# Performance work log

Hardware: AMD Instinct MI355X
Metric: run time of the kernel (lower is better)

The kernel has to match this reference:

```python
import jax, jax.numpy as jnp
import numpy as np

NUM_PHONES = 39
BLANK = NUM_PHONES  # blank appended as last class
NEG = -1e30  # finite stand-in for -inf (log-space)


def ctc_loss(lp, targets, input_lengths, target_lengths, blank):
    """lp: (T, B, C) log-probs. Returns torch-style CTCLoss(reduction='mean', zero_infinity=True)."""
    T, B, C = lp.shape
    L = targets.shape[1]
    S = 2 * L + 1
    # extended label sequence: blank, l1, blank, l2, ..., blank
    ext = jnp.full((B, S), blank, dtype=targets.dtype).at[:, 1::2].set(targets)
    ext_m2 = jnp.concatenate([jnp.full((B, 2), blank, dtype=ext.dtype), ext[:, :-2]], axis=1)
    skip = (ext != blank) & (ext != ext_m2)  # (B, S) allow s-2 transition
    # per-step emission log-probs gathered at extended labels: (T, B, S)
    emit = jnp.take_along_axis(lp, jnp.broadcast_to(ext[None], (T, B, S)), axis=2)

    alpha0 = jnp.full((B, S), NEG, dtype=lp.dtype)
    alpha0 = alpha0.at[:, 0].set(emit[0, :, 0]).at[:, 1].set(emit[0, :, 1])
    pad1 = jnp.full((B, 1), NEG, dtype=lp.dtype)
    pad2 = jnp.full((B, 2), NEG, dtype=lp.dtype)

    def step(alpha, xs):
        emit_t, t = xs
        a1 = jnp.concatenate([pad1, alpha[:, :-1]], axis=1)
        a2 = jnp.where(skip, jnp.concatenate([pad2, alpha[:, :-2]], axis=1), NEG)
        m = jnp.maximum(jnp.maximum(alpha, a1), a2)
        new = m + jnp.log(jnp.exp(alpha - m) + jnp.exp(a1 - m) + jnp.exp(a2 - m)) + emit_t
        new = jnp.where((t < input_lengths)[:, None], new, alpha)  # freeze past length
        return new, None

    alpha, _ = jax.lax.scan(step, alpha0, (emit[1:], jnp.arange(1, T)))
    end = 2 * target_lengths  # index of final blank in extended sequence
    a_blank = jnp.take_along_axis(alpha, end[:, None], axis=1)[:, 0]
    a_label = jnp.take_along_axis(alpha, (end - 1)[:, None], axis=1)[:, 0]
    loss_b = -jnp.logaddexp(a_blank, a_label)
    loss_b = jnp.where(loss_b > 1e29, 0.0, loss_b)  # zero_infinity
    return jnp.mean(loss_b / target_lengths.astype(lp.dtype))


def setup_inputs() -> dict:
    B, T, H, L = 32, 2000, 512, 200
    C = NUM_PHONES + 1
    key = jax.random.key(0)
    k1, k2, k3 = jax.random.split(key, 3)
    hidden = jax.random.normal(k1, (B, T, H), dtype=jnp.float32)
    W = jax.random.normal(k2, (C, H), dtype=jnp.float32) / np.sqrt(H)
    b = jnp.zeros((C,), dtype=jnp.float32)
    targets = jax.random.randint(k3, (B, L), 0, NUM_PHONES, dtype=jnp.int32)
    input_lengths = jnp.full((B,), T, dtype=jnp.int32)
    target_lengths = jnp.full((B,), L, dtype=jnp.int32)
    return {"hidden": hidden, "W": W, "b": b, "targets": targets,
            "input_lengths": input_lengths, "target_lengths": target_lengths}


def reference(hidden, W, b, targets, input_lengths, target_lengths):
    # dropout is identity in eval mode
    logits = jnp.einsum('bth,ch->btc', hidden, W) + b
    log_prob = jax.nn.log_softmax(logits, axis=-1).transpose(1, 0, 2)  # (T, B, C)
    loss = ctc_loss(log_prob, targets, input_lengths, target_lengths, BLANK)
    return (log_prob, loss)
```

## Files before the change

### kernel.cpp

```cpp
#include <hip/hip_runtime.h>
#include <hip/hip_bf16.h>


#define BB 32
#define TT 2000
#define HH 512
#define CC 40
#define LL 200
#define NEGV -1e30f

typedef __attribute__((ext_vector_type(8))) short short8;
typedef __attribute__((ext_vector_type(4))) float f32x4;

__device__ __forceinline__ unsigned short f2bf(float f) {
    unsigned u = __float_as_uint(f);
    u = u + 0x7FFFu + ((u >> 16) & 1u);
    return (unsigned short)(u >> 16);
}

__device__ __forceinline__ double dshr1(double x) {
    int lo = __double2loint(x), hi = __double2hiint(x);
    lo = __builtin_amdgcn_update_dpp(0, lo, 0x138, 0xF, 0xF, false);
    hi = __builtin_amdgcn_update_dpp(0, hi, 0x138, 0xF, 0xF, false);
    return __hiloint2double(hi, lo);
}

__global__ void k0_wconv(const float* __restrict__ W, short* __restrict__ wbf) {
    const int idx = blockIdx.x * 256 + threadIdx.x;
    if (idx < 48 * HH) {
        const int n = idx >> 9, k = idx & (HH - 1);
        wbf[idx] = (n < CC) ? (short)f2bf(W[n * HH + k]) : (short)0;
    }
}

__global__ __launch_bounds__(256) void k1_mfma(
    const float* __restrict__ hidden,
    const short* __restrict__ wbf,
    const float* __restrict__ bias,
    float* __restrict__ out,
    float* __restrict__ P)
{
    const int tid = threadIdx.x, lane = tid & 63, wv = tid >> 6;
    const int quad = lane >> 4, mcol = lane & 15;
    const int r0 = (blockIdx.x * 4 + wv) * 16;

    const float* aptr = hidden + (size_t)(r0 + mcol) * HH + quad * 8;
    const short* b0p = wbf + (0 * 16 + mcol) * HH + quad * 8;
    const short* b1p = wbf + (1 * 16 + mcol) * HH + quad * 8;
    const short* b2p = wbf + (2 * 16 + mcol) * HH + quad * 8;

    f32x4 acc0 = {0.f, 0.f, 0.f, 0.f};
    f32x4 acc1 = {0.f, 0.f, 0.f, 0.f};
    f32x4 acc2 = {0.f, 0.f, 0.f, 0.f};

    #pragma unroll 2
    for (int kc = 0; kc < 16; ++kc) {
        const float4 al = *(const float4*)(aptr + kc * 32);
        const float4 ah = *(const float4*)(aptr + kc * 32 + 4);
        short8 af;
        af[0] = f2bf(al.x); af[1] = f2bf(al.y); af[2] = f2bf(al.z); af[3] = f2bf(al.w);
        af[4] = f2bf(ah.x); af[5] = f2bf(ah.y); af[6] = f2bf(ah.z); af[7] = f2bf(ah.w);
        const short8 bf0 = *(const short8*)(b0p + kc * 32);
        const short8 bf1 = *(const short8*)(b1p + kc * 32);
        const short8 bf2 = *(const short8*)(b2p + kc * 32);
        acc0 = __builtin_amdgcn_mfma_f32_16x16x32_bf16(af, bf0, acc0, 0, 0, 0);
        acc1 = __builtin_amdgcn_mfma_f32_16x16x32_bf16(af, bf1, acc1, 0, 0, 0);
        acc2 = __builtin_amdgcn_mfma_f32_16x16x32_bf16(af, bf2, acc2, 0, 0, 0);
    }

    const float bz0 = bias[mcol];
    const float bz1 = bias[16 + mcol];
    const float bz2 = (mcol < 8) ? bias[32 + mcol] : 0.0f;
    float L0[4], L1[4], L2[4], lse[4];
    #pragma unroll
    for (int j = 0; j < 4; ++j) {
        L0[j] = acc0[j] + bz0;
        L1[j] = acc1[j] + bz1;
        L2[j] = (mcol < 8) ? (acc2[j] + bz2) : NEGV;
    }
    #pragma unroll
    for (int j = 0; j < 4; ++j) {
        float m = fmaxf(fmaxf(L0[j], L1[j]), L2[j]);
        #pragma unroll
        for (int o = 1; o < 16; o <<= 1) m = fmaxf(m, __shfl_xor(m, o, 64));
        float s = __expf(L0[j] - m) + __expf(L1[j] - m)
                + ((mcol < 8) ? __expf(L2[j] - m) : 0.0f);
        #pragma unroll
        for (int o = 1; o < 16; o <<= 1) s += __shfl_xor(s, o, 64);
        lse[j] = m + __logf(s);
    }
    #pragma unroll
    for (int j = 0; j < 4; ++j) {
        const int r = r0 + quad * 4 + j;
        const int b = r / TT, t = r - b * TT;
        float* op = out + ((size_t)t * BB + b) * CC;
        float* pp = P + (size_t)r * CC;
        const float v0 = L0[j] - lse[j];
        const float v1 = L1[j] - lse[j];
        op[mcol]      = v0;  pp[mcol]      = __expf(v0);
        op[16 + mcol] = v1;  pp[16 + mcol] = __expf(v1);
        if (mcol < 8) {
            const float v2 = L2[j] - lse[j];
            op[32 + mcol] = v2;  pp[32 + mcol] = __expf(v2);
        }
    }
}

__global__ __launch_bounds__(64) void k2_fast(
    const float* __restrict__ P,
    const int* __restrict__ targets,
    const int* __restrict__ input_lengths,
    const int* __restrict__ target_lengths,
    float* __restrict__ loss_ws)
{
    const int b = blockIdx.x, l = threadIdx.x;
    const int len = input_lengths[b];
    const int tl  = target_lengths[b];

    int cls[4]; double sk[4];
    #pragma unroll
    for (int j = 0; j < 4; ++j) {
        const int idx = 4 * l + j;
        int c = CC - 1; double skv = 0.0;
        if (idx < tl) {
            c = targets[b * LL + idx];
            if (idx == 0) skv = 1.0;
            else skv = (c != targets[b * LL + idx - 1]) ? 1.0 : 0.0;
        }
        cls[j] = c; sk[j] = skv;
    }
    const int off0 = cls[0], off1 = cls[1], off2 = cls[2], off3 = cls[3];

    const float* rowb = P + (size_t)b * TT * CC;

    double a0, a1, a2, a3, a4, a5, a6, a7;
    {
        const float pb0 = rowb[CC - 1];
        const float pl0 = rowb[off0];
        a0 = (l == 0) ? (double)pb0 : 0.0;
        a1 = (l == 0) ? (double)pl0 : 0.0;
        a2 = a3 = a4 = a5 = a6 = a7 = 0.0;
    }

    float g0[5][8], g1[5][8];
    auto prefetch = [&](float (&g)[5][8]) {
        #pragma unroll
        for (int u = 0; u < 8; ++u) {
            const float* row = rowb + u * CC;
            g[0][u] = row[off0];
            g[1][u] = row[off1];
            g[2][u] = row[off2];
            g[3][u] = row[off3];
            g[4][u] = row[CC - 1];
        }
        rowb += 8 * CC;
    };
    prefetch(g0);

    double logscale = 0.0;

    auto step = [&](float e1f, float e3f, float e5f, float e7f, float bef) {
        const double be = (double)bef;
        const double p7 = dshr1(a7);
        const double n0 = (a0 + p7) * be;
        const double n1 = (a1 + fma(sk[0], p7, a0)) * (double)e1f;
        const double n2 = (a2 + a1) * be;
        const double n3 = (a3 + fma(sk[1], a1, a2)) * (double)e3f;
        const double n4 = (a4 + a3) * be;
        const double n5 = (a5 + fma(sk[2], a3, a4)) * (double)e5f;
        const double n6 = (a6 + a5) * be;
        const double n7 = (a7 + fma(sk[3], a5, a6)) * (double)e7f;
        a0 = n0; a1 = n1; a2 = n2; a3 = n3;
        a4 = n4; a5 = n5; a6 = n6; a7 = n7;
    };
    auto run8f = [&](const float (&g)[5][8], int ufirst) {
        #pragma unroll
        for (int u = 0; u < 8; ++u)
            if (u >= ufirst)
                step(g[0][u], g[1][u], g[2][u], g[3][u], g[4][u]);
    };
    auto run8c = [&](const float (&g)[5][8], int tbase, int ufirst) {
        #pragma unroll
        for (int u = 0; u < 8; ++u)
            if (u >= ufirst && tbase + u < len)
                step(g[0][u], g[1][u], g[2][u], g[3][u], g[4][u]);
    };
    auto rescale = [&]() {
        int h = __double2hiint(a0);
        int h1 = __double2hiint(a1); h = (h1 > h) ? h1 : h;
        h1 = __double2hiint(a2);     h = (h1 > h) ? h1 : h;
        h1 = __double2hiint(a3);     h = (h1 > h) ? h1 : h;
        h1 = __double2hiint(a4);     h = (h1 > h) ? h1 : h;
        h1 = __double2hiint(a5);     h = (h1 > h) ? h1 : h;
        h1 = __double2hiint(a6);     h = (h1 > h) ? h1 : h;
        h1 = __double2hiint(a7);     h = (h1 > h) ? h1 : h;
        #pragma unroll
        for (int o = 1; o < 64; o <<= 1) {
            const int hx = __shfl_xor(h, o, 64);
            h = (hx > h) ? hx : h;
        }
        if (h > 0) {
            const int be_ = h >> 20;
            const int ex  = be_ - 1022;
            const double sf = __hiloint2double((2045 - be_) << 20, 0);
            a0 *= sf; a1 *= sf; a2 *= sf; a3 *= sf;
            a4 *= sf; a5 *= sf; a6 *= sf; a7 *= sf;
            logscale += (double)ex * 0.6931471805599453;
        }
    };

    for (int it = 0; it < 125; ++it) {
        const int t = 16 * it;
        prefetch(g1);
        if (t + 16 <= len) {
            run8f(g0, (it == 0) ? 1 : 0);
            if (it < 124) prefetch(g0);
            run8f(g1, 0);
        } else {
            run8c(g0, t, (it == 0) ? 1 : 0);
            if (it < 124) prefetch(g0);
            run8c(g1, t + 8, 0);
        }
        if (it & 1) rescale();
    }

    double contrib = 0.0;
    const int send = 2 * tl;
    #pragma unroll
    for (int i = 0; i < 8; ++i) {
        const int s = 8 * l + i;
        const double av = (i == 0) ? a0 : (i == 1) ? a1 : (i == 2) ? a2 :
                          (i == 3) ? a3 : (i == 4) ? a4 : (i == 5) ? a5 :
                          (i == 6) ? a6 : a7;
        if (s == send || s == send - 1) contrib += av;
    }
    #pragma unroll
    for (int o = 32; o > 0; o >>= 1) contrib += __shfl_xor(contrib, o, 64);

    if (l == 0) {
        double lb = 0.0;
        if (contrib > 0.0) lb = -(log(contrib) + logscale);
        if (lb > 1e29) lb = 0.0;
        loss_ws[b] = (float)(lb / (double)tl);
    }
}

__global__ void k3_reduce(const float* __restrict__ ws, float* __restrict__ loss_out)
{
    if (threadIdx.x == 0 && blockIdx.x == 0) {
        float sum = 0.0f;
        #pragma unroll
        for (int b = 0; b < BB; ++b) sum += ws[b];
        *loss_out = sum / (float)BB;
    }
}

__global__ __launch_bounds__(256) void k1_lds(
    const float* __restrict__ hidden, const float* __restrict__ W,
    const float* __restrict__ bias, float* __restrict__ out)
{
    __shared__ float Wl[CC * 256];
    float4* Wl4 = (float4*)Wl;
    const int tid = threadIdx.x;
    const int r = blockIdx.x * blockDim.x + tid;
    const float4* __restrict__ h4 = (const float4*)(hidden + (size_t)r * HH);
    const float4* __restrict__ W4g = (const float4*)W;
    float acc[CC];
    #pragma unroll
    for (int c = 0; c < CC; ++c) acc[c] = 0.0f;
    for (int kc = 0; kc < 2; ++kc) {
        __syncthreads();
        #pragma unroll
        for (int i = 0; i < 10; ++i) {
            const int idx = tid + i * 256;
            const int c = idx >> 6, j4 = idx & 63;
            Wl4[idx] = W4g[c * 128 + kc * 64 + j4];
        }
        __syncthreads();
        #pragma unroll 2
        for (int k4 = 0; k4 < 64; ++k4) {
            const float4 h = h4[kc * 64 + k4];
            #pragma unroll
            for (int c = 0; c < CC; ++c) {
                const float4 w = Wl4[c * 64 + k4];
                acc[c] = fmaf(h.x, w.x, fmaf(h.y, w.y,
                         fmaf(h.z, w.z, fmaf(h.w, w.w, acc[c]))));
            }
        }
    }
    #pragma unroll
    for (int c = 0; c < CC; ++c) acc[c] += bias[c];
    float mx = acc[0];
    #pragma unroll
    for (int c = 1; c < CC; ++c) mx = fmaxf(mx, acc[c]);
    float s = 0.0f;
    #pragma unroll
    for (int c = 0; c < CC; ++c) s += __expf(acc[c] - mx);
    const float lse = mx + __logf(s);
    const int b = r / TT, t = r - b * TT;
    float4* __restrict__ o4 = (float4*)(out + ((size_t)t * BB + b) * CC);
    #pragma unroll
    for (int c4 = 0; c4 < CC / 4; ++c4) {
        float4 v;
        v.x = acc[4 * c4 + 0] - lse; v.y = acc[4 * c4 + 1] - lse;
        v.z = acc[4 * c4 + 2] - lse; v.w = acc[4 * c4 + 3] - lse;
        o4[c4] = v;
    }
}

__device__ __forceinline__ float bperm(int byteaddr, float v) {
    return __int_as_float(__builtin_amdgcn_ds_bpermute(byteaddr, __float_as_int(v)));
}

__global__ __launch_bounds__(64) void k2_legacy(
    const float* __restrict__ lp, const int* __restrict__ targets,
    const int* __restrict__ input_lengths, const int* __restrict__ target_lengths,
    float* __restrict__ ws)
{
    const int b = blockIdx.x, lane = threadIdx.x;
    const int len = input_lengths[b];
    const int tl = target_lengths[b];
    const int S = 2 * tl + 1;
    int cad[7]; double skf[7];
    #pragma unroll
    for (int i = 0; i < 7; ++i) {
        const int s = 7 * lane + i;
        int cls = 63; double sk = 0.0;
        if (s < S) {
            if (s & 1) {
                cls = targets[b * LL + (s >> 1)];
                if (s >= 3) sk = (cls != targets[b * LL + ((s - 3) >> 1)]) ? 1.0 : 0.0;
                else sk = 1.0;
            } else cls = CC - 1;
        }
        cad[i] = cls * 4; skf[i] = sk;
    }
    const double lane0m = (lane == 0) ? 0.0 : 1.0;
    const int lc = (lane < CC) ? lane : (CC - 1);
    const size_t rowstride = (size_t)BB * CC;
    const float* lprow = lp + (size_t)b * CC + lc;
    double a0, a1, a2, a3, a4, a5, a6;
    {
        const float v0 = lprow[0];
        const float e = (lane < CC) ? __expf(v0) : 0.0f;
        a0 = (lane == 0) ? (double)bperm(cad[0], e) : 0.0;
        a1 = (lane == 0) ? (double)bperm(cad[1], e) : 0.0;
        a2 = a3 = a4 = a5 = a6 = 0.0;
    }
    float Pr[8];
    #pragma unroll
    for (int u = 0; u < 8; ++u) Pr[u] = lprow[(size_t)(1 + u) * rowstride];
    double logscale = 0.0;
    auto step = [&](int t, float pv) {
        const float ef = (lane < CC) ? __expf(pv) : 0.0f;
        const double e0 = (double)bperm(cad[0], ef), e1 = (double)bperm(cad[1], ef);
        const double e2 = (double)bperm(cad[2], ef), e3 = (double)bperm(cad[3], ef);
        const double e4 = (double)bperm(cad[4], ef), e5 = (double)bperm(cad[5], ef);
        const double e6 = (double)bperm(cad[6], ef);
        const double pl1 = __shfl_up(a6, 1, 64) * lane0m;
        const double pl2 = __shfl_up(a5, 1, 64) * lane0m;
        const double n0 = (a0 + fma(skf[0], pl2, pl1)) * e0;
        const double n1 = (a1 + fma(skf[1], pl1, a0)) * e1;
        const double n2 = (a2 + fma(skf[2], a0, a1)) * e2;
        const double n3 = (a3 + fma(skf[3], a1, a2)) * e3;
        const double n4 = (a4 + fma(skf[4], a2, a3)) * e4;
        const double n5 = (a5 + fma(skf[5], a3, a4)) * e5;
        const double n6 = (a6 + fma(skf[6], a4, a5)) * e6;
        if (t < len) { a0 = n0; a1 = n1; a2 = n2; a3 = n3; a4 = n4; a5 = n5; a6 = n6; }
    };
    auto rescale = [&]() {
        double m = fmax(fmax(fmax(a0, a1), fmax(a2, a3)), fmax(fmax(a4, a5), a6));
        #pragma unroll
        for (int o = 32; o > 0; o >>= 1) m = fmax(m, __shfl_xor(m, o, 64));
        if (m > 0.0) {
            const double inv = 1.0 / m;
            a0 *= inv; a1 *= inv; a2 *= inv; a3 *= inv; a4 *= inv; a5 *= inv; a6 *= inv;
            logscale += (double)__logf((float)m);
        }
    };
    for (int it = 0; it < 249; ++it) {
        const int t = 1 + it * 8, tb = t + 8;
        const float* pf = lprow + (size_t)tb * rowstride;
        float q[8];
        #pragma unroll
        for (int u = 0; u < 8; ++u) q[u] = (tb + u < TT) ? pf[(size_t)u * rowstride] : 0.0f;
        #pragma unroll
        for (int u = 0; u < 8; ++u) step(t + u, Pr[u]);
        rescale();
        #pragma unroll
        for (int u = 0; u < 8; ++u) Pr[u] = q[u];
    }
    #pragma unroll
    for (int u = 0; u < 7; ++u) step(1993 + u, Pr[u]);
    double contrib = 0.0;
    #pragma unroll
    for (int i = 0; i < 7; ++i) {
        const int s = 7 * lane + i;
        const double av = (i == 0) ? a0 : (i == 1) ? a1 : (i == 2) ? a2 :
                          (i == 3) ? a3 : (i == 4) ? a4 : (i == 5) ? a5 : a6;
        if (s == 2 * tl || s == 2 * tl - 1) contrib += av;
    }
    #pragma unroll
    for (int o = 32; o > 0; o >>= 1) contrib += __shfl_xor(contrib, o, 64);
    if (lane == 0) {
        double lb = 0.0;
        if (contrib > 0.0) lb = -(log(contrib) + logscale);
        if (lb > 1e29) lb = 0.0;
        ws[b] = (float)(lb / (double)tl);
    }
}

extern "C" void kernel_launch(void* const* d_in, const int* in_sizes, int n_in,
                              void* d_out, int out_size, void* d_ws, size_t ws_size,
                              hipStream_t stream) {
    const float* hidden = (const float*)d_in[0];
    const float* W      = (const float*)d_in[1];
    const float* bias   = (const float*)d_in[2];
    const int* targets  = (const int*)d_in[3];
    const int* in_len   = (const int*)d_in[4];
    const int* tg_len   = (const int*)d_in[5];

    float* out      = (float*)d_out;
    float* loss_out = out + (size_t)TT * BB * CC;

    const size_t PELEMS   = (size_t)BB * CC * TT;
    const size_t WBF_OFF  = PELEMS;
    const size_t LOSS_OFF = PELEMS + (48 * HH * sizeof(short)) / sizeof(float);
    const size_t need     = (LOSS_OFF + BB) * sizeof(float);

    if (ws_size >= need) {
        float* P   = (float*)d_ws;
        short* wbf = (short*)((float*)d_ws + WBF_OFF);
        float* lws = (float*)d_ws + LOSS_OFF;
        k0_wconv<<<dim3(96), dim3(256), 0, stream>>>(W, wbf);
        k1_mfma<<<dim3(1000), dim3(256), 0, stream>>>(hidden, wbf, bias, out, P);
        k2_fast<<<dim3(BB), dim3(64), 0, stream>>>(P, targets, in_len, tg_len, lws);
        k3_reduce<<<dim3(1), dim3(64), 0, stream>>>(lws, loss_out);
    } else {
        float* lws = (float*)d_ws;
        k1_lds<<<dim3((BB * TT) / 256), dim3(256), 0, stream>>>(hidden, W, bias, out);
        k2_legacy<<<dim3(BB), dim3(64), 0, stream>>>(out, targets, in_len, tg_len, lws);
        k3_reduce<<<dim3(1), dim3(64), 0, stream>>>(lws, loss_out);
    }
}
```

Baseline: 411.8 us.

## Stage log-prob chunks through LDS with coalesced double-buffered loads

Replaces per-lane gathered global loads of emission probabilities with coalesced float4 loads of 40-timestep chunks, written to a double-buffered LDS array and read from there by the recurrence. Rescaling now happens once per 40-step chunk instead of every 16 steps. This aims to cut global gather traffic and shuffle overhead. In exchange, LDS read latency now sits in the serial dependency chain, and there is a larger dynamic range between rescales.

```diff
diff --git a/kernel.cpp b/kernel.cpp
--- a/kernel.cpp
+++ b/kernel.cpp
@@ -117,6 +117,8 @@
     const int len = input_lengths[b];
     const int tl  = target_lengths[b];
 
+    __shared__ float ldsP[2][40 * CC];
+
     int cls[4]; double sk[4];
     #pragma unroll
     for (int j = 0; j < 4; ++j) {
@@ -131,31 +133,38 @@
     }
     const int off0 = cls[0], off1 = cls[1], off2 = cls[2], off3 = cls[3];
 
-    const float* rowb = P + (size_t)b * TT * CC;
+    const float* Pb = P + (size_t)b * TT * CC;
+    const int lane4 = l * 4;
+
+    float4 st[6]; float st6;
+    auto stage_load = [&](int chunk) {
+        const float* src = Pb + (size_t)chunk * (40 * CC);
+        #pragma unroll
+        for (int i = 0; i < 6; ++i)
+            st[i] = *(const float4*)(src + i * 256 + lane4);
+        st6 = src[1536 + l];
+    };
+    auto stage_write = [&](int par) {
+        float* dst = ldsP[par];
+        #pragma unroll
+        for (int i = 0; i < 6; ++i)
+            *(float4*)(dst + i * 256 + lane4) = st[i];
+        dst[1536 + l] = st6;
+    };
+
+    stage_load(0);
+    stage_write(0);
 
     double a0, a1, a2, a3, a4, a5, a6, a7;
     {
-        const float pb0 = rowb[CC - 1];
-        const float pl0 = rowb[off0];
+        const float pb0 = ldsP[0][CC - 1];
+        const float pl0 = ldsP[0][off0];
         a0 = (l == 0) ? (double)pb0 : 0.0;
         a1 = (l == 0) ? (double)pl0 : 0.0;
         a2 = a3 = a4 = a5 = a6 = a7 = 0.0;
     }
 
-    float g0[5][8], g1[5][8];
-    auto prefetch = [&](float (&g)[5][8]) {
-        #pragma unroll
-        for (int u = 0; u < 8; ++u) {
-            const float* row = rowb + u * CC;
-            g[0][u] = row[off0];
-            g[1][u] = row[off1];
-            g[2][u] = row[off2];
-            g[3][u] = row[off3];
-            g[4][u] = row[CC - 1];
-        }
-        rowb += 8 * CC;
-    };
-    prefetch(g0);
+    stage_load(1);
 
     double logscale = 0.0;
 
@@ -173,17 +182,8 @@
         a0 = n0; a1 = n1; a2 = n2; a3 = n3;
         a4 = n4; a5 = n5; a6 = n6; a7 = n7;
     };
-    auto run8f = [&](const float (&g)[5][8], int ufirst) {
-        #pragma unroll
-        for (int u = 0; u < 8; ++u)
-            if (u >= ufirst)
-                step(g[0][u], g[1][u], g[2][u], g[3][u], g[4][u]);
-    };
-    auto run8c = [&](const float (&g)[5][8], int tbase, int ufirst) {
-        #pragma unroll
-        for (int u = 0; u < 8; ++u)
-            if (u >= ufirst && tbase + u < len)
-                step(g[0][u], g[1][u], g[2][u], g[3][u], g[4][u]);
+    auto dostep = [&](const float* row) {
+        step(row[off0], row[off1], row[off2], row[off3], row[CC - 1]);
     };
     auto rescale = [&]() {
         int h = __double2hiint(a0);
@@ -209,19 +209,28 @@
         }
     };
 
-    for (int it = 0; it < 125; ++it) {
-        const int t = 16 * it;
-        prefetch(g1);
-        if (t + 16 <= len) {
-            run8f(g0, (it == 0) ? 1 : 0);
-            if (it < 124) prefetch(g0);
-            run8f(g1, 0);
+    for (int c = 0; c < 50; ++c) {
+        const int par = c & 1;
+        const float* buf = ldsP[par];
+        const int tbase = c * 40;
+        if (tbase + 40 <= len) {
+            if (c == 0) {
+                #pragma unroll 8
+                for (int u = 1; u < 40; ++u) dostep(buf + u * CC);
+            } else {
+                #pragma unroll 8
+                for (int u = 0; u < 40; ++u) dostep(buf + u * CC);
+            }
         } else {
-            run8c(g0, t, (it == 0) ? 1 : 0);
-            if (it < 124) prefetch(g0);
-            run8c(g1, t + 8, 0);
-        }
-        if (it & 1) rescale();
+            const int u0 = (c == 0) ? 1 : 0;
+            for (int u = u0; u < 40; ++u)
+                if (tbase + u < len) dostep(buf + u * CC);
+        }
+        rescale();
+        if (c < 49) {
+            stage_write(par ^ 1);
+            if (c < 48) stage_load(c + 2);
+        }
     }
 
     double contrib = 0.0;
```

New measurement: 384.1 us. -6.7%, faster.
